# Performance work log

Measured on AMD Instinct MI355X. Metric: run time of the kernel, lower is better.

## Reference

```python
import jax, jax.numpy as jnp
import numpy as np

B, T = 512, 512
VOCAB, EMB, DEC = 30001, 512, 128
MAX_OOVS = 50


def setup_inputs() -> dict:
    key = jax.random.key(0)
    ks = jax.random.split(key, 24)
    rn = lambda k, shp, s=0.05: (jax.random.normal(k, shp, dtype=jnp.float32) * s)
    emb = rn(ks[0], (VOCAB, EMB), 1.0).at[0].set(0.0)  # padding_idx=0
    return {
        'h_i': jax.random.normal(ks[1], (B, T, DEC), dtype=jnp.float32),
        'h_prev': jax.random.normal(ks[2], (B, DEC), dtype=jnp.float32),
        'c_prev': jax.random.normal(ks[3], (B, DEC), dtype=jnp.float32),
        'context_vector': jax.random.normal(ks[4], (B, DEC), dtype=jnp.float32),
        'coverage': jax.random.uniform(ks[5], (B, T), dtype=jnp.float32),
        'emb': emb,
        'W_ih': rn(ks[6], (4 * DEC, EMB)), 'W_hh': rn(ks[7], (4 * DEC, DEC)),
        'b_ih': rn(ks[8], (4 * DEC,)), 'b_hh': rn(ks[9], (4 * DEC,)),
        'W1_w': rn(ks[10], (EMB, EMB + DEC)), 'W1_b': rn(ks[11], (EMB,)),
        'W2_w': rn(ks[12], (1, 3 * DEC + EMB)), 'W2_b': rn(ks[13], (1,)),
        'V1_w': rn(ks[14], (3 * DEC, 2 * DEC)), 'V1_b': rn(ks[15], (3 * DEC,)),
        'V2_w': rn(ks[16], (VOCAB, 3 * DEC)), 'V2_b': rn(ks[17], (VOCAB,)),
        'Wh_w': rn(ks[18], (DEC, DEC)),
        'Ws_w': rn(ks[19], (DEC, 2 * DEC)), 'Ws_b': rn(ks[20], (DEC,)),
        'Wc_w': rn(ks[21], (DEC, 1)),
        'V_w': rn(ks[22], (1, DEC)),
        'x': jax.random.randint(ks[23], (B, 1), 0, VOCAB),
        'code_ext': jax.random.randint(jax.random.fold_in(key, 99), (B, T), 0, VOCAB + MAX_OOVS),
        'max_oovs': MAX_OOVS,
    }


def reference(h_i, h_prev, c_prev, context_vector, coverage, emb,
              W_ih, W_hh, b_ih, b_hh, W1_w, W1_b, W2_w, W2_b,
              V1_w, V1_b, V2_w, V2_b, Wh_w, Ws_w, Ws_b, Wc_w, V_w,
              x, code_ext, max_oovs):
    xe = emb[x[:, 0]]                                        # [B, EMB]
    x1 = jnp.concatenate([xe, context_vector], 1) @ W1_w.T + W1_b
    # LSTMCell (gate order i, f, g, o)
    gates = x1 @ W_ih.T + b_ih + h_prev @ W_hh.T + b_hh
    i, f, g, o = jnp.split(gates, 4, axis=1)
    c = jax.nn.sigmoid(f) * c_prev + jax.nn.sigmoid(i) * jnp.tanh(g)
    h = jax.nn.sigmoid(o) * jnp.tanh(c)
    s_t = jnp.concatenate([h, c], 1)                         # [B, 2*DEC]
    # Bahdanau attention with coverage
    enc_f = h_i @ Wh_w.T                                     # [B, T, DEC]
    dec_f = (s_t @ Ws_w.T + Ws_b)[:, None, :]
    cov_f = coverage[:, :, None] * Wc_w[:, 0][None, None, :]
    e_t = jnp.tanh(enc_f + dec_f + cov_f) @ V_w[0]           # [B, T]
    a_t = jax.nn.softmax(e_t, axis=-1)
    coverage_new = coverage + a_t
    ctx = jnp.einsum('bt,btd->bd', a_t, h_i)                 # [B, DEC]
    # vocab distribution
    pv = jnp.concatenate([h, ctx], 1) @ V1_w.T + V1_b
    pv = jax.nn.softmax(pv @ V2_w.T + V2_b, axis=1)          # [B, VOCAB]
    p_gen = jax.nn.sigmoid(jnp.concatenate([ctx, s_t, xe], 1) @ W2_w.T + W2_b)  # [B,1]
    pv = p_gen * pv
    attn_dist = (1.0 - p_gen) * a_t
    pv_ext = jnp.concatenate([pv, jnp.zeros((pv.shape[0], max_oovs), pv.dtype)], axis=-1)
    rows = jnp.arange(pv.shape[0])[:, None]
    final_dist = pv_ext.at[rows, code_ext].add(attn_dist)    # scatter_add copy mechanism
    return (final_dist, attn_dist, h, c, coverage_new, ctx)
```

## Files before the change

kernel.cpp:

```cpp
#include <hip/hip_runtime.h>
#include <math.h>

#define B_    512
#define T_    512
#define DEC_  128
#define EMB_  512
#define VOC_  30001
#define VEXT_ 30051

typedef float f32x4 __attribute__((ext_vector_type(4)));
typedef short s16x4 __attribute__((ext_vector_type(4)));
typedef short s16x8 __attribute__((ext_vector_type(8)));
typedef unsigned u32x4 __attribute__((ext_vector_type(4)));

#define L2E 1.4426950408889634f

__device__ __forceinline__ float sigmoid_f(float x) {
  return __builtin_amdgcn_rcpf(1.f + exp2f(-x * L2E));
}
__device__ __forceinline__ float tanh_f(float x) {
  return 1.f - 2.f * __builtin_amdgcn_rcpf(exp2f(x * (2.f * L2E)) + 1.f);
}
__device__ __forceinline__ short f2bf(float f) {
  unsigned u = __builtin_bit_cast(unsigned, f);
  u += 0x7FFFu + ((u >> 16) & 1u);
  return (short)(u >> 16);
}
__device__ __forceinline__ float bf2f(unsigned short h) {
  return __builtin_bit_cast(float, (unsigned)h << 16);
}
__device__ __forceinline__ unsigned pk_bf16(float lo, float hi) {
  unsigned r;
  asm("v_cvt_pk_bf16_f32 %0, %1, %2" : "=v"(r) : "v"(lo), "v"(hi));
  return r;
}
__device__ __forceinline__ s16x8 pk8(f32x4 w0, f32x4 w1) {
  u32x4 r;
  r[0] = pk_bf16(w0[0], w0[1]); r[1] = pk_bf16(w0[2], w0[3]);
  r[2] = pk_bf16(w1[0], w1[1]); r[3] = pk_bf16(w1[2], w1[3]);
  return __builtin_bit_cast(s16x8, r);
}
__device__ __forceinline__ unsigned short* logit_row(float* outF, int b) {
  size_t byteoff = ((size_t)b * VEXT_ * 4 + 127) & ~(size_t)127;
  return (unsigned short*)((char*)outF + byteoff);
}
__device__ __forceinline__ void gload_lds16(const void* g, void* l) {
  __builtin_amdgcn_global_load_lds(
      (const __attribute__((address_space(1))) void*)g,
      (__attribute__((address_space(3))) void*)l, 16, 0, 0);
}

__global__ __launch_bounds__(256) void k0_prep32(
    const float* __restrict__ Whw, unsigned short* __restrict__ bw) {
  const int t = threadIdx.x;
#pragma unroll
  for (int i = 0; i < 8; ++i) {
    int p = t + 256 * i;
    int f = p >> 6, l = p & 63;
    int nf = f >> 2, kf = f & 3;
    int row = nf * 16 + (l & 15);
    int col = kf * 32 + (l >> 4) * 8;
    const float* src = Whw + row * 128 + col;
    f32x4 w0 = *(const f32x4*)src;
    f32x4 w1 = *(const f32x4*)(src + 4);
    *(s16x8*)&bw[p * 8] = pk8(w0, w1);
  }
}

__global__ __launch_bounds__(256) void k0b_prepv2h(
    const float* __restrict__ V2w, unsigned short* __restrict__ v2bh) {
  int p = blockIdx.x * 256 + threadIdx.x;
  int row = p / 48;
  int k = (p - row * 48) * 8;
  s16x8 bb;
  if (row < VOC_) {
    const float* src = V2w + (size_t)row * 384 + k;
    f32x4 w0 = *(const f32x4*)src;
    f32x4 w1 = *(const f32x4*)(src + 4);
    bb = pk8(w0, w1);
  } else {
    bb = (s16x8){0, 0, 0, 0, 0, 0, 0, 0};
  }
  *(s16x8*)&v2bh[(size_t)p * 8] = bb;
}

__global__ __launch_bounds__(256) void k1_x1(
    const float* __restrict__ emb, const int* __restrict__ x,
    const float* __restrict__ ctxp, const float* __restrict__ W1w,
    const float* __restrict__ W1b, float* __restrict__ x1) {
  __shared__ float As[32][33];
  __shared__ float Ws[32][33];
  const int tid = threadIdx.x;
  const int f0 = blockIdx.x * 32, b0 = blockIdx.y * 32;
  const int row = tid >> 3, seg = tid & 7;
  const int tx = tid & 15, ty = tid >> 4;
  float a00 = 0.f, a01 = 0.f, a10 = 0.f, a11 = 0.f;
  for (int k0 = 0; k0 < 640; k0 += 32) {
    int k = k0 + seg * 4;
    f32x4 av;
    if (k < 512) {
      int xb = x[b0 + row];
      av = *(const f32x4*)(emb + xb * 512 + k);
    } else {
      av = *(const f32x4*)(ctxp + (b0 + row) * 128 + (k - 512));
    }
    As[row][seg * 4 + 0] = av[0]; As[row][seg * 4 + 1] = av[1];
    As[row][seg * 4 + 2] = av[2]; As[row][seg * 4 + 3] = av[3];
    f32x4 wv = *(const f32x4*)(W1w + (f0 + row) * 640 + k);
    Ws[row][seg * 4 + 0] = wv[0]; Ws[row][seg * 4 + 1] = wv[1];
    Ws[row][seg * 4 + 2] = wv[2]; Ws[row][seg * 4 + 3] = wv[3];
    __syncthreads();
#pragma unroll
    for (int kk = 0; kk < 32; ++kk) {
      float v0 = As[ty * 2][kk], v1 = As[ty * 2 + 1][kk];
      float w0 = Ws[tx * 2][kk], w1 = Ws[tx * 2 + 1][kk];
      a00 += v0 * w0; a01 += v0 * w1; a10 += v1 * w0; a11 += v1 * w1;
    }
    __syncthreads();
  }
  int fo = f0 + tx * 2, bo = b0 + ty * 2;
  x1[bo * 512 + fo]           = a00 + W1b[fo];
  x1[bo * 512 + fo + 1]       = a01 + W1b[fo + 1];
  x1[(bo + 1) * 512 + fo]     = a10 + W1b[fo];
  x1[(bo + 1) * 512 + fo + 1] = a11 + W1b[fo + 1];
}

__global__ __launch_bounds__(256) void k2_gates(
    const float* __restrict__ x1, const float* __restrict__ hprev,
    const float* __restrict__ Wih, const float* __restrict__ Whh,
    const float* __restrict__ bih, const float* __restrict__ bhh,
    float* __restrict__ gates) {
  __shared__ float As[32][33];
  __shared__ float Ws[32][33];
  const int tid = threadIdx.x;
  const int f0 = blockIdx.x * 32, b0 = blockIdx.y * 32;
  const int row = tid >> 3, seg = tid & 7;
  const int tx = tid & 15, ty = tid >> 4;
  float a00 = 0.f, a01 = 0.f, a10 = 0.f, a11 = 0.f;
  for (int k0 = 0; k0 < 640; k0 += 32) {
    int k = k0 + seg * 4;
    f32x4 av, wv;
    if (k < 512) {
      av = *(const f32x4*)(x1 + (b0 + row) * 512 + k);
      wv = *(const f32x4*)(Wih + (f0 + row) * 512 + k);
    } else {
      av = *(const f32x4*)(hprev + (b0 + row) * 128 + (k - 512));
      wv = *(const f32x4*)(Whh + (f0 + row) * 128 + (k - 512));
    }
    As[row][seg * 4 + 0] = av[0]; As[row][seg * 4 + 1] = av[1];
    As[row][seg * 4 + 2] = av[2]; As[row][seg * 4 + 3] = av[3];
    Ws[row][seg * 4 + 0] = wv[0]; Ws[row][seg * 4 + 1] = wv[1];
    Ws[row][seg * 4 + 2] = wv[2]; Ws[row][seg * 4 + 3] = wv[3];
    __syncthreads();
#pragma unroll
    for (int kk = 0; kk < 32; ++kk) {
      float v0 = As[ty * 2][kk], v1 = As[ty * 2 + 1][kk];
      float w0 = Ws[tx * 2][kk], w1 = Ws[tx * 2 + 1][kk];
      a00 += v0 * w0; a01 += v0 * w1; a10 += v1 * w0; a11 += v1 * w1;
    }
    __syncthreads();
  }
  int fo = f0 + tx * 2, bo = b0 + ty * 2;
  gates[bo * 512 + fo]           = a00 + bih[fo] + bhh[fo];
  gates[bo * 512 + fo + 1]       = a01 + bih[fo + 1] + bhh[fo + 1];
  gates[(bo + 1) * 512 + fo]     = a10 + bih[fo] + bhh[fo];
  gates[(bo + 1) * 512 + fo + 1] = a11 + bih[fo + 1] + bhh[fo + 1];
}

__global__ __launch_bounds__(128) void k3_lstm(
    const float* __restrict__ gates, const float* __restrict__ cprev,
    const float* __restrict__ Wsw, const float* __restrict__ Wsb,
    float* __restrict__ out_h, float* __restrict__ out_c,
    float* __restrict__ decf) {
  __shared__ float st[256];
  int b = blockIdx.x, d = threadIdx.x;
  const float* g = gates + b * 512;
  float iv = sigmoid_f(g[d]);
  float fv = sigmoid_f(g[128 + d]);
  float gv = tanh_f(g[256 + d]);
  float ov = sigmoid_f(g[384 + d]);
  float c = fv * cprev[b * 128 + d] + iv * gv;
  float h = ov * tanh_f(c);
  out_h[b * 128 + d] = h;
  out_c[b * 128 + d] = c;
  st[d] = h; st[128 + d] = c;
  __syncthreads();
  float acc = Wsb[d];
  const float* wr = Wsw + d * 256;
#pragma unroll 4
  for (int k = 0; k < 256; ++k) acc += st[k] * wr[k];
  decf[b * 128 + d] = acc;
}

__global__ __launch_bounds__(512) void k45_attn(
    const float* __restrict__ h_i, const unsigned short* __restrict__ bw,
    const float* __restrict__ decf, const float* __restrict__ cov,
    const float* __restrict__ Wcw, const float* __restrict__ Vw,
    float* __restrict__ a_t, float* __restrict__ cov_out,
    float* __restrict__ ctx_out) {
  __shared__ unsigned short whl[16384];
  __shared__ float sm[512];
  __shared__ float red[16][128];
  __shared__ float wred[8];
  const int b = blockIdx.x;
  const int tid = threadIdx.x;
  const int wv = tid >> 6, lane = tid & 63;
  const int lm = lane & 15, lg = lane >> 4;
  const int t0w = wv * 64;

#pragma unroll
  for (int i = 0; i < 4; ++i)
    gload_lds16(&bw[(tid + i * 512) * 8], &whl[(tid + i * 512) * 8]);

  float dec_v[8], vw_v[8], wc_v[8];
#pragma unroll
  for (int nf = 0; nf < 8; ++nf) {
    dec_v[nf] = decf[b * 128 + nf * 16 + lm];
    vw_v[nf]  = Vw[nf * 16 + lm];
    wc_v[nf]  = Wcw[nf * 16 + lm];
  }
  __syncthreads();

  const f32x4 zf4 = {0.f, 0.f, 0.f, 0.f};
  const float* abase = h_i + ((size_t)(b * 512 + t0w + lm)) * 128 + lg * 8;

  f32x4 r0, r1, r2, r3, r4, r5, r6, r7;
  f32x4 cv_raw;
#define K45_LOADC(c)                                            \
  do {                                                          \
    const float* p_ = abase + (size_t)(c) * 16 * 128;           \
    r0 = *(const f32x4*)(p_ + 0);   r1 = *(const f32x4*)(p_ + 4);   \
    r2 = *(const f32x4*)(p_ + 32);  r3 = *(const f32x4*)(p_ + 36);  \
    r4 = *(const f32x4*)(p_ + 64);  r5 = *(const f32x4*)(p_ + 68);  \
    r6 = *(const f32x4*)(p_ + 96);  r7 = *(const f32x4*)(p_ + 100); \
    cv_raw = *(const f32x4*)&cov[b * 512 + t0w + (c) * 16 + lg * 4];\
  } while (0)

  K45_LOADC(0);
#pragma unroll
  for (int c = 0; c < 4; ++c) {
    s16x8 pk0 = pk8(r0, r1), pk1 = pk8(r2, r3);
    s16x8 pk2 = pk8(r4, r5), pk3 = pk8(r6, r7);
    f32x4 cov4 = cv_raw;
    if (c < 3) K45_LOADC(c + 1);

    float e4[4] = {0.f, 0.f, 0.f, 0.f};
#pragma unroll
    for (int nf = 0; nf < 8; ++nf) {
      s16x8 b0_ = *(const s16x8*)&whl[((nf * 4 + 0) * 64 + lane) * 8];
      s16x8 b1_ = *(const s16x8*)&whl[((nf * 4 + 1) * 64 + lane) * 8];
      s16x8 b2_ = *(const s16x8*)&whl[((nf * 4 + 2) * 64 + lane) * 8];
      s16x8 b3_ = *(const s16x8*)&whl[((nf * 4 + 3) * 64 + lane) * 8];
      f32x4 cc = zf4;
      cc = __builtin_amdgcn_mfma_f32_16x16x32_bf16(pk0, b0_, cc, 0, 0, 0);
      cc = __builtin_amdgcn_mfma_f32_16x16x32_bf16(pk1, b1_, cc, 0, 0, 0);
      cc = __builtin_amdgcn_mfma_f32_16x16x32_bf16(pk2, b2_, cc, 0, 0, 0);
      cc = __builtin_amdgcn_mfma_f32_16x16x32_bf16(pk3, b3_, cc, 0, 0, 0);
#pragma unroll
      for (int r = 0; r < 4; ++r) {
        float v = cc[r] + dec_v[nf] + cov4[r] * wc_v[nf];
        e4[r] += vw_v[nf] * tanh_f(v);
      }
    }
#pragma unroll
    for (int i = 0; i < 4; ++i) {
      float v = e4[i];
      v += __shfl_xor(v, 1); v += __shfl_xor(v, 2);
      v += __shfl_xor(v, 4); v += __shfl_xor(v, 8);
      e4[i] = v;
    }
    if (lm == 0) {
#pragma unroll
      for (int r = 0; r < 4; ++r)
        sm[t0w + c * 16 + lg * 4 + r] = e4[r];
    }
  }
#undef K45_LOADC
  __syncthreads();

  float e = sm[tid];
  float m = e;
  for (int off = 32; off; off >>= 1) m = fmaxf(m, __shfl_xor(m, off));
  if (lane == 0) wred[wv] = m;
  __syncthreads();
  float M = wred[0];
#pragma unroll
  for (int i = 1; i < 8; ++i) M = fmaxf(M, wred[i]);
  float ex = exp2f((e - M) * L2E);
  float s = ex;
  for (int off = 32; off; off >>= 1) s += __shfl_xor(s, off);
  __syncthreads();
  if (lane == 0) wred[wv] = s;
  __syncthreads();
  float S = 0.f;
#pragma unroll
  for (int i = 0; i < 8; ++i) S += wred[i];
  float a = ex * __builtin_amdgcn_rcpf(S);
  a_t[b * 512 + tid] = a;
  cov_out[b * 512 + tid] = cov[b * 512 + tid] + a;
  sm[tid] = a;
  __syncthreads();

  int j = tid & 31, tg = tid >> 5;
  const float* hb = h_i + (size_t)b * 65536 + j * 4;
  f32x4 acc = zf4;
#pragma unroll 8
  for (int t = tg; t < 512; t += 16) {
    float av = sm[t];
    f32x4 hv = *(const f32x4*)(hb + (size_t)t * 128);
    acc += hv * av;
  }
  *(f32x4*)&red[tg][j * 4] = acc;
  __syncthreads();
  if (tid < 128) {
    float sa = 0.f;
#pragma unroll
    for (int g = 0; g < 16; ++g) sa += red[g][tid];
    ctx_out[b * 128 + tid] = sa;
  }
}

__global__ __launch_bounds__(256) void k6_pv1_pgen(
    const float* __restrict__ out_h, const float* __restrict__ out_c,
    const float* __restrict__ ctx, const float* __restrict__ emb,
    const int* __restrict__ x, const float* __restrict__ V1w,
    const float* __restrict__ V1b, const float* __restrict__ W2w,
    const float* __restrict__ W2b, const float* __restrict__ a_t,
    unsigned short* __restrict__ pv1bf, float* __restrict__ pgen,
    float* __restrict__ attn_out) {
  __shared__ float cat[896];
  __shared__ float wr_[4];
  int b = blockIdx.x, tid = threadIdx.x;
  if (tid < 128) {
    cat[tid] = ctx[b * 128 + tid];
    cat[128 + tid] = out_h[b * 128 + tid];
  } else {
    int q = tid - 128;
    cat[256 + q] = out_c[b * 128 + q];
  }
  int xb = x[b];
  for (int k = tid; k < 512; k += 256) cat[384 + k] = emb[xb * 512 + k];
  __syncthreads();
  for (int f = tid; f < 384; f += 256) {
    const float* w = V1w + f * 256;
    float acc = V1b[f];
#pragma unroll 4
    for (int k = 0; k < 256; ++k) {
      float av = (k < 128) ? cat[128 + k] : cat[k - 128];
      acc += av * w[k];
    }
    pv1bf[b * 384 + f] = (unsigned short)f2bf(acc);
  }
  float p = 0.f;
  for (int k = tid; k < 896; k += 256) p += cat[k] * W2w[k];
  for (int off = 32; off; off >>= 1) p += __shfl_xor(p, off);
  if ((tid & 63) == 0) wr_[tid >> 6] = p;
  __syncthreads();
  float pg = sigmoid_f(wr_[0] + wr_[1] + wr_[2] + wr_[3] + W2b[0]);
  if (tid == 0) pgen[b] = pg;
  float om = 1.f - pg;
  attn_out[b * 512 + tid]       = om * a_t[b * 512 + tid];
  attn_out[b * 512 + 256 + tid] = om * a_t[b * 512 + 256 + tid];
}

__global__ __launch_bounds__(256) void k7_vocab(
    const unsigned short* __restrict__ pv1bf, const unsigned short* __restrict__ v2bh,
    const float* __restrict__ V2b, float* __restrict__ outF) {
  __shared__ char smem[33280];
  unsigned short* Al = (unsigned short*)smem;
  unsigned short* Bl = (unsigned short*)(smem + 16384);
  const int bx = blockIdx.x;
  const int rp = bx & 3, cp = bx >> 2;
  const int r0 = rp * 128, c0 = cp * 128;
  const int tid = threadIdx.x;
  const int wv = tid >> 6, lane = tid & 63;
  const int lm = lane & 15, lg = lane >> 4;
  const int rh2 = wv >> 1, ch = wv & 1;

  const f32x4 zf4 = {0.f, 0.f, 0.f, 0.f};
  f32x4 acc[4][4];
#pragma unroll
  for (int m = 0; m < 4; ++m)
#pragma unroll
    for (int nf = 0; nf < 4; ++nf) acc[m][nf] = zf4;

  for (int ks = 0; ks < 6; ++ks) {
#pragma unroll
    for (int i = 0; i < 4; ++i) {
      int fi = wv * 4 + i;
      int rt = fi >> 1, kf = fi & 1;
      const unsigned short* sa =
          pv1bf + (r0 + rt * 16 + lm) * 384 + ks * 64 + kf * 32 + lg * 8;
      gload_lds16(sa, &Al[fi * 512 + lane * 8]);
      const unsigned short* sb =
          v2bh + (size_t)(c0 + rt * 16 + lm) * 384 + ks * 64 + kf * 32 + lg * 8;
      gload_lds16(sb, &Bl[fi * 512 + lane * 8]);
    }
    __syncthreads();
#pragma unroll
    for (int kf = 0; kf < 2; ++kf) {
      s16x8 a[4];
#pragma unroll
      for (int m = 0; m < 4; ++m)
        a[m] = *(const s16x8*)&Al[(((rh2 * 4 + m) * 2) + kf) * 512 + lane * 8];
#pragma unroll
      for (int nf = 0; nf < 4; ++nf) {
        s16x8 bfr = *(const s16x8*)&Bl[(((ch * 4 + nf) * 2) + kf) * 512 + lane * 8];
#pragma unroll
        for (int m = 0; m < 4; ++m)
          acc[m][nf] = __builtin_amdgcn_mfma_f32_16x16x32_bf16(a[m], bfr, acc[m][nf], 0, 0, 0);
      }
    }
    __syncthreads();
  }

  const int cw0 = c0 + ch * 64;
  float bias[4];
#pragma unroll
  for (int nf = 0; nf < 4; ++nf) {
    int col = cw0 + nf * 16 + lm;
    bias[nf] = (col < VOC_) ? V2b[col] : 0.f;
  }

  float* T = (float*)smem + wv * 2080;
  const int rq = lane >> 4, cq = lane & 15;
#pragma unroll
  for (int p = 0; p < 2; ++p) {
#pragma unroll
    for (int mm = 0; mm < 2; ++mm) {
      int m = p * 2 + mm;
#pragma unroll
      for (int nf = 0; nf < 4; ++nf)
#pragma unroll
        for (int r = 0; r < 4; ++r)
          T[(mm * 16 + lg * 4 + r) * 65 + nf * 16 + lm] = acc[m][nf][r] + bias[nf];
    }
#pragma unroll
    for (int it = 0; it < 8; ++it) {
      int trow = it * 4 + rq;
      f32x4 vv = *(const f32x4*)&T[trow * 65 + cq * 4];
      s16x4 hb;
      hb[0] = f2bf(vv[0]); hb[1] = f2bf(vv[1]); hb[2] = f2bf(vv[2]); hb[3] = f2bf(vv[3]);
      int orow = r0 + rh2 * 64 + p * 32 + trow;
      unsigned short* dst = logit_row(outF, orow);
      *(s16x4*)&dst[cw0 + cq * 4] = hb;
    }
  }
}

__global__ __launch_bounds__(256) void k7_vocab_fb(
    const unsigned short* __restrict__ pv1bf, const float* __restrict__ V2w,
    const float* __restrict__ V2b, float* __restrict__ outF) {
  __shared__ float lt[4][32 * 65];
  const int q = blockIdx.x;
  const int nb = ((q >> 4) << 3) + (q & 7);
  const int rh = (q >> 3) & 1;
  if (nb >= 469) return;
  const int v0 = nb * 64;
  const int tid = threadIdx.x;
  const int wv = tid >> 6, lane = tid & 63;
  const int lm = lane & 15, lg = lane >> 4;
  const int r0 = rh * 256 + wv * 64;

  const f32x4 zf4 = {0.f, 0.f, 0.f, 0.f};
  f32x4 acc[4][4];
#pragma unroll
  for (int m = 0; m < 4; ++m)
#pragma unroll
    for (int nf = 0; nf < 4; ++nf) acc[m][nf] = zf4;

  int vrow[4]; bool vok[4];
#pragma unroll
  for (int nf = 0; nf < 4; ++nf) {
    int v = v0 + nf * 16 + lm;
    vok[nf] = (v < VOC_);
    vrow[nf] = vok[nf] ? v : (VOC_ - 1);
  }

#pragma unroll
  for (int kf = 0; kf < 12; ++kf) {
    s16x8 afr[4];
#pragma unroll
    for (int m = 0; m < 4; ++m)
      afr[m] = *(const s16x8*)&pv1bf[(r0 + m * 16 + lm) * 384 + kf * 32 + lg * 8];
    s16x8 bfr[4];
#pragma unroll
    for (int nf = 0; nf < 4; ++nf) {
      const float* p = V2w + (size_t)vrow[nf] * 384 + kf * 32 + lg * 8;
      f32x4 w0 = *(const f32x4*)p;
      f32x4 w1 = *(const f32x4*)(p + 4);
      if (!vok[nf]) { w0 = zf4; w1 = zf4; }
      bfr[nf] = pk8(w0, w1);
    }
#pragma unroll
    for (int m = 0; m < 4; ++m)
#pragma unroll
      for (int nf = 0; nf < 4; ++nf)
        acc[m][nf] = __builtin_amdgcn_mfma_f32_16x16x32_bf16(afr[m], bfr[nf], acc[m][nf], 0, 0, 0);
  }

  float bias[4];
#pragma unroll
  for (int nf = 0; nf < 4; ++nf)
    bias[nf] = vok[nf] ? V2b[v0 + nf * 16 + lm] : 0.f;

  float* T = lt[wv];
  const int rq = lane >> 4, cq = lane & 15;
#pragma unroll
  for (int p = 0; p < 2; ++p) {
#pragma unroll
    for (int mm = 0; mm < 2; ++mm) {
      int m = p * 2 + mm;
#pragma unroll
      for (int nf = 0; nf < 4; ++nf)
#pragma unroll
        for (int r = 0; r < 4; ++r)
          T[(mm * 16 + lg * 4 + r) * 65 + nf * 16 + lm] = acc[m][nf][r] + bias[nf];
    }
#pragma unroll
    for (int it = 0; it < 8; ++it) {
      int trow = it * 4 + rq;
      f32x4 vv = *(const f32x4*)&T[trow * 65 + cq * 4];
      s16x4 hb;
      hb[0] = f2bf(vv[0]); hb[1] = f2bf(vv[1]); hb[2] = f2bf(vv[2]); hb[3] = f2bf(vv[3]);
      int orow = r0 + p * 32 + trow;
      unsigned short* dst = logit_row(outF, orow);
      *(s16x4*)&dst[v0 + cq * 4] = hb;
    }
  }
}

#define K8_IT 30

__global__ __launch_bounds__(1024) void k8_final(
    const float* __restrict__ pgen, const int* __restrict__ code_ext,
    const float* __restrict__ attn, float* __restrict__ outF) {
  __shared__ float lm_[16], ls_[16];
  const int b = blockIdx.x, tid = threadIdx.x;
  float* row = outF + (size_t)b * VEXT_;
  const unsigned short* lrow = logit_row(outF, b);

  float lv[K8_IT];
#pragma unroll
  for (int i = 0; i < K8_IT; ++i) {
    int v = tid + i * 1024;
    lv[i] = (v < VOC_) ? bf2f(lrow[v]) : -3.4e38f;
  }
  float m = lv[0];
#pragma unroll
  for (int i = 1; i < K8_IT; ++i) m = fmaxf(m, lv[i]);
  for (int off = 32; off; off >>= 1) m = fmaxf(m, __shfl_xor(m, off));
  if ((tid & 63) == 0) lm_[tid >> 6] = m;
  __syncthreads();
  float M = lm_[0];
#pragma unroll
  for (int i = 1; i < 16; ++i) M = fmaxf(M, lm_[i]);
  float s = 0.f;
#pragma unroll
  for (int i = 0; i < K8_IT; ++i) {
    lv[i] = exp2f((lv[i] - M) * L2E);
    s += lv[i];
  }
  for (int off = 32; off; off >>= 1) s += __shfl_xor(s, off);
  if ((tid & 63) == 0) ls_[tid >> 6] = s;
  __syncthreads();
  float S = 0.f;
#pragma unroll
  for (int i = 0; i < 16; ++i) S += ls_[i];
  float pm = pgen[b] / S;
#pragma unroll
  for (int i = 0; i < K8_IT; ++i) {
    int v = tid + i * 1024;
    if (v < VOC_) row[v] = pm * lv[i];
  }
  if (tid < 50) row[VOC_ + tid] = 0.f;
  __syncthreads();
  if (tid < 512) {
    int idx = code_ext[b * 512 + tid];
    __hip_atomic_fetch_add(&row[idx], attn[b * 512 + tid],
                           __ATOMIC_RELAXED, __HIP_MEMORY_SCOPE_WORKGROUP);
  }
}

extern "C" void kernel_launch(void* const* d_in, const int* in_sizes, int n_in,
                              void* d_out, int out_size, void* d_ws, size_t ws_size,
                              hipStream_t stream) {
  (void)in_sizes; (void)n_in; (void)out_size;
  const float* h_i    = (const float*)d_in[0];
  const float* h_prev = (const float*)d_in[1];
  const float* c_prev = (const float*)d_in[2];
  const float* ctxp   = (const float*)d_in[3];
  const float* cov    = (const float*)d_in[4];
  const float* emb    = (const float*)d_in[5];
  const float* Wih    = (const float*)d_in[6];
  const float* Whh    = (const float*)d_in[7];
  const float* bih    = (const float*)d_in[8];
  const float* bhh    = (const float*)d_in[9];
  const float* W1w    = (const float*)d_in[10];
  const float* W1b    = (const float*)d_in[11];
  const float* W2w    = (const float*)d_in[12];
  const float* W2b    = (const float*)d_in[13];
  const float* V1w    = (const float*)d_in[14];
  const float* V1b    = (const float*)d_in[15];
  const float* V2w    = (const float*)d_in[16];
  const float* V2b    = (const float*)d_in[17];
  const float* Whw    = (const float*)d_in[18];
  const float* Wsw    = (const float*)d_in[19];
  const float* Wsb    = (const float*)d_in[20];
  const float* Wcw    = (const float*)d_in[21];
  const float* Vw     = (const float*)d_in[22];
  const int*   x      = (const int*)d_in[23];
  const int*   code   = (const int*)d_in[24];

  float* ws    = (float*)d_ws;
  float* x1    = ws;
  float* gates = ws + 262144;
  float* decf  = ws + 524288;
  unsigned short* bw = (unsigned short*)(ws + 589824);
  float* a_t   = ws + 851968;
  unsigned short* pv1bf = (unsigned short*)(ws + 1114112);
  float* pgen  = ws + 1212416;
  unsigned short* v2bh = (unsigned short*)(ws + 1212928);
  const size_t WS_NEEDED = (size_t)(1212928 + 5775360) * 4;
  const bool use_v6 = (ws_size >= WS_NEEDED);

  float* outF  = (float*)d_out;
  float* attn  = outF + (size_t)512 * VEXT_;
  float* o_h   = attn + 262144;
  float* o_c   = o_h + 65536;
  float* o_cov = o_c + 65536;
  float* o_ctx = o_cov + 262144;

  k0_prep32<<<1, 256, 0, stream>>>(Whw, bw);
  if (use_v6) k0b_prepv2h<<<5640, 256, 0, stream>>>(V2w, v2bh);
  k1_x1<<<dim3(16, 16), 256, 0, stream>>>(emb, x, ctxp, W1w, W1b, x1);
  k2_gates<<<dim3(16, 16), 256, 0, stream>>>(x1, h_prev, Wih, Whh, bih, bhh, gates);
  k3_lstm<<<512, 128, 0, stream>>>(gates, c_prev, Wsw, Wsb, o_h, o_c, decf);
  k45_attn<<<512, 512, 0, stream>>>(h_i, bw, decf, cov, Wcw, Vw, a_t, o_cov, o_ctx);
  k6_pv1_pgen<<<512, 256, 0, stream>>>(o_h, o_c, o_ctx, emb, x, V1w, V1b, W2w, W2b,
                                       a_t, pv1bf, pgen, attn);
  if (use_v6)
    k7_vocab<<<940, 256, 0, stream>>>(pv1bf, v2bh, V2b, outF);
  else
    k7_vocab_fb<<<944, 256, 0, stream>>>(pv1bf, V2w, V2b, outF);
  k8_final<<<512, 1024, 0, stream>>>(pgen, code, attn, outF);
}
```

Measured before the change: 237.1 us.

## Fuse attention context into score pass and move V1 projection to MFMA GEMM

The attention kernel now builds the context vector during the same pass that computes scores. It uses an upper-bound shift, the sum of |V_w|, in place of a max-reduction, so the h_i row already held in bf16 registers is weighted immediately and the second read of h_i is gone. The per-batch scalar V1 projection is moved into a separate bf16 MFMA tiled GEMM fed by a bf16 [h,ctx] buffer written by the LSTM and attention kernels, with a prep kernel converting V1_w to bf16. This drops one max-reduction and a global re-read, but the context is now accumulated from bf16-rounded h_i and adds two kernel launches.

```diff
diff --git a/kernel.cpp b/kernel.cpp
--- a/kernel.cpp
+++ b/kernel.cpp
@@ -28,6 +28,9 @@
 }
 __device__ __forceinline__ float bf2f(unsigned short h) {
   return __builtin_bit_cast(float, (unsigned)h << 16);
+}
+__device__ __forceinline__ float bitsf(unsigned u) {
+  return __builtin_bit_cast(float, u);
 }
 __device__ __forceinline__ unsigned pk_bf16(float lo, float hi) {
   unsigned r;
@@ -82,6 +85,14 @@
     bb = (s16x8){0, 0, 0, 0, 0, 0, 0, 0};
   }
   *(s16x8*)&v2bh[(size_t)p * 8] = bb;
+}
+
+__global__ __launch_bounds__(256) void k0c_prepv1(
+    const float* __restrict__ V1w, unsigned short* __restrict__ v1bh) {
+  int p = blockIdx.x * 256 + threadIdx.x;
+  int row = p >> 5, k = (p & 31) * 8;
+  const float* src = V1w + row * 256 + k;
+  *(s16x8*)&v1bh[p * 8] = pk8(*(const f32x4*)src, *(const f32x4*)(src + 4));
 }
 
 __global__ __launch_bounds__(256) void k1_x1(
@@ -171,7 +182,7 @@
     const float* __restrict__ gates, const float* __restrict__ cprev,
     const float* __restrict__ Wsw, const float* __restrict__ Wsb,
     float* __restrict__ out_h, float* __restrict__ out_c,
-    float* __restrict__ decf) {
+    float* __restrict__ decf, unsigned short* __restrict__ hc_bf) {
   __shared__ float st[256];
   int b = blockIdx.x, d = threadIdx.x;
   const float* g = gates + b * 512;
@@ -183,6 +194,7 @@
   float h = ov * tanh_f(c);
   out_h[b * 128 + d] = h;
   out_c[b * 128 + d] = c;
+  hc_bf[b * 256 + d] = (unsigned short)f2bf(h);
   st[d] = h; st[128 + d] = c;
   __syncthreads();
   float acc = Wsb[d];
@@ -197,11 +209,12 @@
     const float* __restrict__ decf, const float* __restrict__ cov,
     const float* __restrict__ Wcw, const float* __restrict__ Vw,
     float* __restrict__ a_t, float* __restrict__ cov_out,
-    float* __restrict__ ctx_out) {
+    float* __restrict__ ctx_out, unsigned short* __restrict__ hc_bf) {
   __shared__ unsigned short whl[16384];
   __shared__ float sm[512];
-  __shared__ float red[16][128];
+  __shared__ float red[8][128];
   __shared__ float wred[8];
+  __shared__ float dls[128], vls[128], wls[128];
   const int b = blockIdx.x;
   const int tid = threadIdx.x;
   const int wv = tid >> 6, lane = tid & 63;
@@ -211,21 +224,29 @@
 #pragma unroll
   for (int i = 0; i < 4; ++i)
     gload_lds16(&bw[(tid + i * 512) * 8], &whl[(tid + i * 512) * 8]);
-
-  float dec_v[8], vw_v[8], wc_v[8];
-#pragma unroll
-  for (int nf = 0; nf < 8; ++nf) {
-    dec_v[nf] = decf[b * 128 + nf * 16 + lm];
-    vw_v[nf]  = Vw[nf * 16 + lm];
-    wc_v[nf]  = Wcw[nf * 16 + lm];
-  }
-  __syncthreads();
+  if (tid < 128) {
+    dls[tid] = decf[b * 128 + tid];
+    vls[tid] = Vw[tid];
+    wls[tid] = Wcw[tid];
+  }
+  __syncthreads();
+
+  const volatile float* vlp = vls;
+  const volatile float* dlp = dls;
+  const volatile float* wlp = wls;
+  float E1 = 0.f;
+#pragma unroll
+  for (int nf = 0; nf < 8; ++nf) E1 += fabsf(vlp[nf * 16 + lm]);
+  E1 += __shfl_xor(E1, 1); E1 += __shfl_xor(E1, 2);
+  E1 += __shfl_xor(E1, 4); E1 += __shfl_xor(E1, 8);
 
   const f32x4 zf4 = {0.f, 0.f, 0.f, 0.f};
   const float* abase = h_i + ((size_t)(b * 512 + t0w + lm)) * 128 + lg * 8;
 
   f32x4 r0, r1, r2, r3, r4, r5, r6, r7;
   f32x4 cv_raw;
+  f32x4 c0 = zf4, c1 = zf4, c2 = zf4, c3 = zf4;
+  f32x4 c4 = zf4, c5 = zf4, c6 = zf4, c7 = zf4;
 #define K45_LOADC(c)                                            \
   do {                                                          \
     const float* p_ = abase + (size_t)(c) * 16 * 128;           \
@@ -235,6 +256,14 @@
     r6 = *(const f32x4*)(p_ + 96);  r7 = *(const f32x4*)(p_ + 100); \
     cv_raw = *(const f32x4*)&cov[b * 512 + t0w + (c) * 16 + lg * 4];\
   } while (0)
+#define K45_ACC(ca, cb, pk)                                         \
+  do {                                                              \
+    u32x4 q_ = __builtin_bit_cast(u32x4, pk);                       \
+    ca[0] += w * bitsf(q_[0] << 16); ca[1] += w * bitsf(q_[0] & 0xFFFF0000u); \
+    ca[2] += w * bitsf(q_[1] << 16); ca[3] += w * bitsf(q_[1] & 0xFFFF0000u); \
+    cb[0] += w * bitsf(q_[2] << 16); cb[1] += w * bitsf(q_[2] & 0xFFFF0000u); \
+    cb[2] += w * bitsf(q_[3] << 16); cb[3] += w * bitsf(q_[3] & 0xFFFF0000u); \
+  } while (0)
 
   K45_LOADC(0);
 #pragma unroll
@@ -247,6 +276,9 @@
     float e4[4] = {0.f, 0.f, 0.f, 0.f};
 #pragma unroll
     for (int nf = 0; nf < 8; ++nf) {
+      float dv = dlp[nf * 16 + lm];
+      float vw = vlp[nf * 16 + lm];
+      float wc = wlp[nf * 16 + lm];
       s16x8 b0_ = *(const s16x8*)&whl[((nf * 4 + 0) * 64 + lane) * 8];
       s16x8 b1_ = *(const s16x8*)&whl[((nf * 4 + 1) * 64 + lane) * 8];
       s16x8 b2_ = *(const s16x8*)&whl[((nf * 4 + 2) * 64 + lane) * 8];
@@ -258,8 +290,8 @@
       cc = __builtin_amdgcn_mfma_f32_16x16x32_bf16(pk3, b3_, cc, 0, 0, 0);
 #pragma unroll
       for (int r = 0; r < 4; ++r) {
-        float v = cc[r] + dec_v[nf] + cov4[r] * wc_v[nf];
-        e4[r] += vw_v[nf] * tanh_f(v);
+        float v = cc[r] + dv + cov4[r] * wc;
+        e4[r] += vw * tanh_f(v);
       }
     }
 #pragma unroll
@@ -274,60 +306,151 @@
       for (int r = 0; r < 4; ++r)
         sm[t0w + c * 16 + lg * 4 + r] = e4[r];
     }
+    int src = (lm >> 2) << 4;
+    float s0 = __shfl(e4[0], src), s1 = __shfl(e4[1], src);
+    float s2 = __shfl(e4[2], src), s3 = __shfl(e4[3], src);
+    int rr = lm & 3;
+    float ev = rr == 0 ? s0 : (rr == 1 ? s1 : (rr == 2 ? s2 : s3));
+    float w = exp2f((ev - E1) * L2E);
+    K45_ACC(c0, c1, pk0);
+    K45_ACC(c2, c3, pk1);
+    K45_ACC(c4, c5, pk2);
+    K45_ACC(c6, c7, pk3);
   }
 #undef K45_LOADC
+#undef K45_ACC
+
+#define BFLY(x) { x += __shfl_xor(x, 1); x += __shfl_xor(x, 2); \
+                  x += __shfl_xor(x, 4); x += __shfl_xor(x, 8); }
+#pragma unroll
+  for (int j = 0; j < 4; ++j) {
+    BFLY(c0[j]); BFLY(c1[j]); BFLY(c2[j]); BFLY(c3[j]);
+    BFLY(c4[j]); BFLY(c5[j]); BFLY(c6[j]); BFLY(c7[j]);
+  }
+#undef BFLY
+  if (lm == 0) {
+    float* rw = &red[wv][lg * 8];
+#pragma unroll
+    for (int j = 0; j < 4; ++j) {
+      rw[j] = c0[j];       rw[4 + j] = c1[j];
+      rw[32 + j] = c2[j];  rw[36 + j] = c3[j];
+      rw[64 + j] = c4[j];  rw[68 + j] = c5[j];
+      rw[96 + j] = c6[j];  rw[100 + j] = c7[j];
+    }
+  }
   __syncthreads();
 
   float e = sm[tid];
-  float m = e;
-  for (int off = 32; off; off >>= 1) m = fmaxf(m, __shfl_xor(m, off));
-  if (lane == 0) wred[wv] = m;
-  __syncthreads();
-  float M = wred[0];
-#pragma unroll
-  for (int i = 1; i < 8; ++i) M = fmaxf(M, wred[i]);
-  float ex = exp2f((e - M) * L2E);
-  float s = ex;
+  float w2 = exp2f((e - E1) * L2E);
+  float s = w2;
   for (int off = 32; off; off >>= 1) s += __shfl_xor(s, off);
-  __syncthreads();
   if (lane == 0) wred[wv] = s;
   __syncthreads();
-  float S = 0.f;
-#pragma unroll
-  for (int i = 0; i < 8; ++i) S += wred[i];
-  float a = ex * __builtin_amdgcn_rcpf(S);
+  float S1 = 0.f;
+#pragma unroll
+  for (int i = 0; i < 8; ++i) S1 += wred[i];
+  float rS = __builtin_amdgcn_rcpf(S1);
+  float a = w2 * rS;
   a_t[b * 512 + tid] = a;
   cov_out[b * 512 + tid] = cov[b * 512 + tid] + a;
-  sm[tid] = a;
-  __syncthreads();
-
-  int j = tid & 31, tg = tid >> 5;
-  const float* hb = h_i + (size_t)b * 65536 + j * 4;
-  f32x4 acc = zf4;
-#pragma unroll 8
-  for (int t = tg; t < 512; t += 16) {
-    float av = sm[t];
-    f32x4 hv = *(const f32x4*)(hb + (size_t)t * 128);
-    acc += hv * av;
-  }
-  *(f32x4*)&red[tg][j * 4] = acc;
-  __syncthreads();
   if (tid < 128) {
     float sa = 0.f;
 #pragma unroll
-    for (int g = 0; g < 16; ++g) sa += red[g][tid];
-    ctx_out[b * 128 + tid] = sa;
-  }
-}
-
-__global__ __launch_bounds__(256) void k6_pv1_pgen(
+    for (int g = 0; g < 8; ++g) sa += red[g][tid];
+    float cx = sa * rS;
+    ctx_out[b * 128 + tid] = cx;
+    hc_bf[b * 256 + 128 + tid] = (unsigned short)f2bf(cx);
+  }
+}
+
+__global__ __launch_bounds__(256) void k6a_pv1(
+    const unsigned short* __restrict__ hc_bf, const unsigned short* __restrict__ v1bh,
+    const float* __restrict__ V1b, unsigned short* __restrict__ pv1bf) {
+  __shared__ char smem[33280];
+  unsigned short* Al = (unsigned short*)smem;
+  unsigned short* Bl = (unsigned short*)(smem + 16384);
+  const int bx = blockIdx.x;
+  const int rp = bx & 3, cp = bx >> 2;
+  const int r0 = rp * 128, c0 = cp * 128;
+  const int tid = threadIdx.x;
+  const int wv = tid >> 6, lane = tid & 63;
+  const int lm = lane & 15, lg = lane >> 4;
+  const int rh2 = wv >> 1, ch = wv & 1;
+
+  const f32x4 zf4 = {0.f, 0.f, 0.f, 0.f};
+  f32x4 acc[4][4];
+#pragma unroll
+  for (int m = 0; m < 4; ++m)
+#pragma unroll
+    for (int nf = 0; nf < 4; ++nf) acc[m][nf] = zf4;
+
+  for (int ks = 0; ks < 4; ++ks) {
+#pragma unroll
+    for (int i = 0; i < 4; ++i) {
+      int fi = wv * 4 + i;
+      int rt = fi >> 1, kf = fi & 1;
+      const unsigned short* sa =
+          hc_bf + (r0 + rt * 16 + lm) * 256 + ks * 64 + kf * 32 + lg * 8;
+      gload_lds16(sa, &Al[fi * 512 + lane * 8]);
+      const unsigned short* sb =
+          v1bh + (c0 + rt * 16 + lm) * 256 + ks * 64 + kf * 32 + lg * 8;
+      gload_lds16(sb, &Bl[fi * 512 + lane * 8]);
+    }
+    __syncthreads();
+#pragma unroll
+    for (int kf = 0; kf < 2; ++kf) {
+      s16x8 a[4];
+#pragma unroll
+      for (int m = 0; m < 4; ++m)
+        a[m] = *(const s16x8*)&Al[(((rh2 * 4 + m) * 2) + kf) * 512 + lane * 8];
+#pragma unroll
+      for (int nf = 0; nf < 4; ++nf) {
+        s16x8 bfr = *(const s16x8*)&Bl[(((ch * 4 + nf) * 2) + kf) * 512 + lane * 8];
+#pragma unroll
+        for (int m = 0; m < 4; ++m)
+          acc[m][nf] = __builtin_amdgcn_mfma_f32_16x16x32_bf16(a[m], bfr, acc[m][nf], 0, 0, 0);
+      }
+    }
+    __syncthreads();
+  }
+
+  const int cw0 = c0 + ch * 64;
+  float bias[4];
+#pragma unroll
+  for (int nf = 0; nf < 4; ++nf)
+    bias[nf] = V1b[cw0 + nf * 16 + lm];
+
+  float* T = (float*)smem + wv * 2080;
+  const int rq = lane >> 4, cq = lane & 15;
+#pragma unroll
+  for (int p = 0; p < 2; ++p) {
+#pragma unroll
+    for (int mm = 0; mm < 2; ++mm) {
+      int m = p * 2 + mm;
+#pragma unroll
+      for (int nf = 0; nf < 4; ++nf)
+#pragma unroll
+        for (int r = 0; r < 4; ++r)
+          T[(mm * 16 + lg * 4 + r) * 65 + nf * 16 + lm] = acc[m][nf][r] + bias[nf];
+    }
+#pragma unroll
+    for (int it = 0; it < 8; ++it) {
+      int trow = it * 4 + rq;
+      f32x4 vv = *(const f32x4*)&T[trow * 65 + cq * 4];
+      s16x4 hb;
+      hb[0] = f2bf(vv[0]); hb[1] = f2bf(vv[1]); hb[2] = f2bf(vv[2]); hb[3] = f2bf(vv[3]);
+      int orow = r0 + rh2 * 64 + p * 32 + trow;
+      *(s16x4*)&pv1bf[orow * 384 + cw0 + cq * 4] = hb;
+    }
+  }
+}
+
+__global__ __launch_bounds__(256) void k6b_pgen(
     const float* __restrict__ out_h, const float* __restrict__ out_c,
     const float* __restrict__ ctx, const float* __restrict__ emb,
-    const int* __restrict__ x, const float* __restrict__ V1w,
-    const float* __restrict__ V1b, const float* __restrict__ W2w,
+    const int* __restrict__ x, const float* __restrict__ W2w,
     const float* __restrict__ W2b, const float* __restrict__ a_t,
-    unsigned short* __restrict__ pv1bf, float* __restrict__ pgen,
-    float* __restrict__ attn_out) {
+    float* __restrict__ pgen, float* __restrict__ attn_out) {
   __shared__ float cat[896];
   __shared__ float wr_[4];
   int b = blockIdx.x, tid = threadIdx.x;
@@ -341,16 +464,6 @@
   int xb = x[b];
   for (int k = tid; k < 512; k += 256) cat[384 + k] = emb[xb * 512 + k];
   __syncthreads();
-  for (int f = tid; f < 384; f += 256) {
-    const float* w = V1w + f * 256;
-    float acc = V1b[f];
-#pragma unroll 4
-    for (int k = 0; k < 256; ++k) {
-      float av = (k < 128) ? cat[128 + k] : cat[k - 128];
-      acc += av * w[k];
-    }
-    pv1bf[b * 384 + f] = (unsigned short)f2bf(acc);
-  }
   float p = 0.f;
   for (int k = tid; k < 896; k += 256) p += cat[k] * W2w[k];
   for (int off = 32; off; off >>= 1) p += __shfl_xor(p, off);
@@ -617,6 +730,8 @@
   float* gates = ws + 262144;
   float* decf  = ws + 524288;
   unsigned short* bw = (unsigned short*)(ws + 589824);
+  unsigned short* hc_bf = (unsigned short*)(ws + 598016);
+  unsigned short* v1bh  = (unsigned short*)(ws + 663552);
   float* a_t   = ws + 851968;
   unsigned short* pv1bf = (unsigned short*)(ws + 1114112);
   float* pgen  = ws + 1212416;
@@ -633,12 +748,15 @@
 
   k0_prep32<<<1, 256, 0, stream>>>(Whw, bw);
   if (use_v6) k0b_prepv2h<<<5640, 256, 0, stream>>>(V2w, v2bh);
+  k0c_prepv1<<<48, 256, 0, stream>>>(V1w, v1bh);
   k1_x1<<<dim3(16, 16), 256, 0, stream>>>(emb, x, ctxp, W1w, W1b, x1);
   k2_gates<<<dim3(16, 16), 256, 0, stream>>>(x1, h_prev, Wih, Whh, bih, bhh, gates);
-  k3_lstm<<<512, 128, 0, stream>>>(gates, c_prev, Wsw, Wsb, o_h, o_c, decf);
-  k45_attn<<<512, 512, 0, stream>>>(h_i, bw, decf, cov, Wcw, Vw, a_t, o_cov, o_ctx);
-  k6_pv1_pgen<<<512, 256, 0, stream>>>(o_h, o_c, o_ctx, emb, x, V1w, V1b, W2w, W2b,
-                                       a_t, pv1bf, pgen, attn);
+  k3_lstm<<<512, 128, 0, stream>>>(gates, c_prev, Wsw, Wsb, o_h, o_c, decf, hc_bf);
+  k45_attn<<<512, 512, 0, stream>>>(h_i, bw, decf, cov, Wcw, Vw, a_t, o_cov,
+                                    o_ctx, hc_bf);
+  k6a_pv1<<<12, 256, 0, stream>>>(hc_bf, v1bh, V1b, pv1bf);
+  k6b_pgen<<<512, 256, 0, stream>>>(o_h, o_c, o_ctx, emb, x, W2w, W2b, a_t,
+                                    pgen, attn);
   if (use_v6)
     k7_vocab<<<940, 256, 0, stream>>>(pv1bf, v2bh, V2b, outF);
   else
```

After: 221.7 us (median of 2 runs). -6.5%, faster.
